# Kernel optimization log

Hardware: AMD Instinct MI355X
Metric: run time of the kernel (lower is better)

The kernel has to match this reference:

```python
import jax, jax.numpy as jnp
import numpy as np

NUM_HEADS = 16


def _bayes_w(mu, rho, eps):
    # reparameterized weight sample: w = mu + softplus(rho) * eps
    return mu + jax.nn.softplus(rho) * eps


def setup_inputs() -> dict:
    key = jax.random.key(0)
    ks = jax.random.split(key, 12)
    B, N, C = 4, 2048, 1024
    x = jax.random.normal(ks[0], (B, N, C), jnp.float32)
    w_scale = 0.02
    q_w = jax.random.normal(ks[1], (C, C), jnp.float32) * w_scale
    k_w = jax.random.normal(ks[2], (C, C), jnp.float32) * w_scale
    v_mu = jax.random.normal(ks[3], (C, C), jnp.float32) * w_scale
    v_rho = jax.random.normal(ks[4], (C, C), jnp.float32) * 0.1 - 3.0
    v_eps = jax.random.normal(ks[5], (C, C), jnp.float32)
    proj_mu = jax.random.normal(ks[6], (C, C), jnp.float32) * w_scale
    proj_rho = jax.random.normal(ks[7], (C, C), jnp.float32) * 0.1 - 3.0
    proj_eps = jax.random.normal(ks[8], (C, C), jnp.float32)
    pb_mu = jax.random.normal(ks[9], (C,), jnp.float32) * w_scale
    pb_rho = jax.random.normal(ks[10], (C,), jnp.float32) * 0.1 - 3.0
    pb_eps = jax.random.normal(ks[11], (C,), jnp.float32)
    return {"x": x, "q_w": q_w, "k_w": k_w, "v_mu": v_mu, "v_rho": v_rho,
            "v_eps": v_eps, "proj_mu": proj_mu, "proj_rho": proj_rho,
            "proj_eps": proj_eps, "pb_mu": pb_mu, "pb_rho": pb_rho,
            "pb_eps": pb_eps}


def reference(x, q_w, k_w, v_mu, v_rho, v_eps, proj_mu, proj_rho, proj_eps,
              pb_mu, pb_rho, pb_eps):
    B, N, C = x.shape
    H = NUM_HEADS
    D = C // H
    scale = D ** -0.5
    v_w = _bayes_w(v_mu, v_rho, v_eps)
    # projections (torch Linear: y = x @ W.T)
    q = (x @ q_w.T).reshape(B, N, H, D).transpose(0, 2, 1, 3)  # [B,H,N,D]
    k = (x @ k_w.T).reshape(B, N, H, D).transpose(0, 2, 1, 3)
    v = (x @ v_w.T).reshape(B, N, H, D).transpose(0, 2, 1, 3)
    attn = jax.nn.softmax(jnp.einsum("bhnd,bhmd->bhnm", q * scale, k), axis=-1)
    out = jnp.einsum("bhnm,bhmd->bhnd", attn, v)
    out = out.transpose(0, 2, 1, 3).reshape(B, N, C)
    p_w = _bayes_w(proj_mu, proj_rho, proj_eps)
    p_b = _bayes_w(pb_mu, pb_rho, pb_eps)
    return out @ p_w.T + p_b
```

## Files before the change

kernel.cpp:

```cpp
#include <hip/hip_runtime.h>
#include <hip/hip_bf16.h>
#include <cstdint>
#include <math.h>

typedef __bf16 bf16;
typedef __bf16 bf16x8 __attribute__((ext_vector_type(8)));
typedef __bf16 bf16x4 __attribute__((ext_vector_type(4)));
typedef float  f32x4 __attribute__((ext_vector_type(4)));

#define LOG2E 1.4426950408889634f

#if __has_builtin(__builtin_amdgcn_exp2f)
#define EXP2(x) __builtin_amdgcn_exp2f(x)
#else
#define EXP2(x) exp2f(x)
#endif

#define AS1 __attribute__((address_space(1)))
#define AS3 __attribute__((address_space(3)))

__device__ __forceinline__ void gload_lds16(const bf16* g, bf16* l) {
    __builtin_amdgcn_global_load_lds((AS1 void*)g, (AS3 void*)l, 16, 0, 0);
}

__device__ __forceinline__ float softplus_f(float r) {
    return (r > 15.f) ? r : log1pf(expf(r));
}

#define MFMA16(a, b, c) __builtin_amdgcn_mfma_f32_16x16x32_bf16((a), (b), (c), 0, 0, 0)
#define CFENCE asm volatile("" ::: "memory")

__global__ __launch_bounds__(256)
void prep_kernel(const float* __restrict__ x, bf16* __restrict__ xb,
                 const float* __restrict__ q_w, const float* __restrict__ k_w,
                 bf16* __restrict__ wqkv,
                 const float* __restrict__ v_mu, const float* __restrict__ v_rho,
                 const float* __restrict__ v_eps,
                 const float* __restrict__ p_mu, const float* __restrict__ p_rho,
                 const float* __restrict__ p_eps, bf16* __restrict__ pwb,
                 const float* __restrict__ pb_mu, const float* __restrict__ pb_rho,
                 const float* __restrict__ pb_eps, float* __restrict__ p_b) {
    const int Wsz = 1024 * 1024;
    int blk = blockIdx.x;
    if (blk < 8192) {
        int i = blk * 256 + threadIdx.x;
        float4 v = ((const float4*)x)[i];
        bf16 o[4] = {(bf16)v.x, (bf16)v.y, (bf16)v.z, (bf16)v.w};
        *(uint64_t*)&xb[i * 4] = *(uint64_t*)o;
    } else if (blk < 10240) {
        const float* src = (blk < 9216) ? q_w : k_w;
        bf16* dst = (blk < 9216) ? wqkv : wqkv + Wsz;
        int i = ((blk - 8192) & 1023) * 256 + threadIdx.x;
        float4 v = ((const float4*)src)[i];
        bf16 o[4] = {(bf16)v.x, (bf16)v.y, (bf16)v.z, (bf16)v.w};
        *(uint64_t*)&dst[i * 4] = *(uint64_t*)o;
    } else if (blk < 12288) {
        const bool isv = blk < 11264;
        const float* mu  = isv ? v_mu  : p_mu;
        const float* rho = isv ? v_rho : p_rho;
        const float* eps = isv ? v_eps : p_eps;
        bf16* dst = isv ? wqkv + 2 * Wsz : pwb;
        int i = ((blk - 10240) & 1023) * 256 + threadIdx.x;
        float4 m = ((const float4*)mu)[i];
        float4 r = ((const float4*)rho)[i];
        float4 e = ((const float4*)eps)[i];
        bf16 o[4] = {(bf16)(m.x + softplus_f(r.x) * e.x),
                     (bf16)(m.y + softplus_f(r.y) * e.y),
                     (bf16)(m.z + softplus_f(r.z) * e.z),
                     (bf16)(m.w + softplus_f(r.w) * e.w)};
        *(uint64_t*)&dst[i * 4] = *(uint64_t*)o;
    } else {
        int i = threadIdx.x;
        float4 m = ((const float4*)pb_mu)[i];
        float4 r = ((const float4*)pb_rho)[i];
        float4 e = ((const float4*)pb_eps)[i];
        float4 o;
        o.x = m.x + softplus_f(r.x) * e.x;
        o.y = m.y + softplus_f(r.y) * e.y;
        o.z = m.z + softplus_f(r.z) * e.z;
        o.w = m.w + softplus_f(r.w) * e.w;
        ((float4*)p_b)[i] = o;
    }
}

template <typename OutT, int BL>
__global__ __launch_bounds__(512, 2)
void gemm_8ph(const bf16* __restrict__ A, const bf16* __restrict__ W,
              OutT* __restrict__ C, const float* __restrict__ bias,
              int M, int N, int K, float q_scale, int q_cols) {
    __shared__ __align__(16) char smem[131072];
    bf16* sA = (bf16*)smem;
    bf16* sB = (bf16*)(smem + 65536);
    const int BN = 128 * BL;
    const int SBB = BN * 64;

    const int lane  = threadIdx.x & 63;
    const int wv    = threadIdx.x >> 6;
    const int wr    = wv >> 2;
    const int wc    = wv & 3;
    const int col16 = lane & 15, quad = lane >> 4;

    const int nwg = gridDim.x * gridDim.y;
    int bidl = blockIdx.y * gridDim.x + blockIdx.x;
    if ((nwg & 7) == 0) bidl = (bidl & 7) * (nwg >> 3) + (bidl >> 3);
    const int m0 = (bidl / gridDim.x) * 256;
    const int n0 = (bidl % gridDim.x) * BN;

    const int st_r = lane >> 2;
    const int st_c = ((lane & 3) * 8) ^ (((lane >> 5) & 1) << 4);
    const bf16* Asrc = A + (size_t)(m0 + st_r) * K + st_c;
    const bf16* Bsrc = W + (size_t)(n0 + st_r) * K + st_c;
    const size_t rgK = (size_t)16 * K;

    const int lp = col16 * 32 + ((quad * 8) ^ (((col16 >> 3) & 1) << 4));

    f32x4 acc[2][2][4][BL] = {};
    const int NT = K >> 6;

#define STAGE_A(buf, half, kt) do { \
        const bf16* s_ = Asrc + (size_t)((half) * 8 + wv) * rgK + ((size_t)(kt) << 6); \
        bf16* l_ = &sA[(buf) * 16384 + ((half) * 8 + wv) * 1024]; \
        gload_lds16(s_, l_); gload_lds16(s_ + 32, l_ + 512); } while (0)
#define STAGE_B(buf, half, kt) do { \
        if constexpr (BL == 2) { \
            const bf16* s_ = Bsrc + (size_t)((half) * 8 + wv) * rgK + ((size_t)(kt) << 6); \
            bf16* l_ = &sB[(buf) * SBB + ((half) * 8 + wv) * 1024]; \
            gload_lds16(s_, l_); gload_lds16(s_ + 32, l_ + 512); \
        } else { \
            const int rg_ = wv >> 1, kc_ = wv & 1; \
            const bf16* s_ = Bsrc + (size_t)((half) * 4 + rg_) * rgK + kc_ * 32 + ((size_t)(kt) << 6); \
            gload_lds16(s_, &sB[(buf) * SBB + (((half) * 4 + rg_) * 2 + kc_) * 512]); \
        } } while (0)
#define WAIT_STEADY do { \
        if constexpr (BL == 2) asm volatile("s_waitcnt vmcnt(6)" ::: "memory"); \
        else                   asm volatile("s_waitcnt vmcnt(4)" ::: "memory"); } while (0)

    STAGE_A(0, 0, 0); STAGE_B(0, 0, 0); STAGE_B(0, 1, 0); STAGE_A(0, 1, 0);
    if (NT > 1) { STAGE_A(1, 0, 1); STAGE_B(1, 0, 1); STAGE_B(1, 1, 1); }
    if (NT > 1) WAIT_STEADY;
    else        asm volatile("s_waitcnt vmcnt(0)" ::: "memory");
    __builtin_amdgcn_s_barrier();
    CFENCE;

    bf16x8 afr[4][2], bfr0[BL][2], bfr1[BL][2];

    for (int t = 0; t < NT; ++t) {
        const int d = t & 1;

#pragma unroll
        for (int mm = 0; mm < 4; ++mm)
#pragma unroll
            for (int ks = 0; ks < 2; ++ks)
                afr[mm][ks] = *(const bf16x8*)&sA[d * 16384 + ((2 * mm + wr) * 2 + ks) * 512 + lp];
#pragma unroll
        for (int nn = 0; nn < BL; ++nn)
#pragma unroll
            for (int ks = 0; ks < 2; ++ks)
                bfr0[nn][ks] = *(const bf16x8*)&sB[d * SBB + ((nn * 4 + wc) * 2 + ks) * 512 + lp];
        if (t + 1 < NT) STAGE_A(d ^ 1, 1, t + 1);
        CFENCE; __builtin_amdgcn_s_barrier(); CFENCE;
        __builtin_amdgcn_s_setprio(1);
#pragma unroll
        for (int mm = 0; mm < 4; ++mm)
#pragma unroll
            for (int nn = 0; nn < BL; ++nn) {
                acc[0][0][mm][nn] = MFMA16(afr[mm][0], bfr0[nn][0], acc[0][0][mm][nn]);
                acc[0][0][mm][nn] = MFMA16(afr[mm][1], bfr0[nn][1], acc[0][0][mm][nn]);
            }
        __builtin_amdgcn_s_setprio(0);
        CFENCE; __builtin_amdgcn_s_barrier(); CFENCE;

#pragma unroll
        for (int nn = 0; nn < BL; ++nn)
#pragma unroll
            for (int ks = 0; ks < 2; ++ks)
                bfr1[nn][ks] = *(const bf16x8*)&sB[d * SBB + ((4 * BL + nn * 4 + wc) * 2 + ks) * 512 + lp];
        if (t + 2 < NT) STAGE_A(d, 0, t + 2);
        CFENCE; __builtin_amdgcn_s_barrier(); CFENCE;
        __builtin_amdgcn_s_setprio(1);
#pragma unroll
        for (int mm = 0; mm < 4; ++mm)
#pragma unroll
            for (int nn = 0; nn < BL; ++nn) {
                acc[0][1][mm][nn] = MFMA16(afr[mm][0], bfr1[nn][0], acc[0][1][mm][nn]);
                acc[0][1][mm][nn] = MFMA16(afr[mm][1], bfr1[nn][1], acc[0][1][mm][nn]);
            }
        __builtin_amdgcn_s_setprio(0);
        CFENCE; __builtin_amdgcn_s_barrier(); CFENCE;

#pragma unroll
        for (int mm = 0; mm < 4; ++mm)
#pragma unroll
            for (int ks = 0; ks < 2; ++ks)
                afr[mm][ks] = *(const bf16x8*)&sA[d * 16384 + ((8 + 2 * mm + wr) * 2 + ks) * 512 + lp];
        if (t + 2 < NT) STAGE_B(d, 0, t + 2);
        CFENCE; __builtin_amdgcn_s_barrier(); CFENCE;
        __builtin_amdgcn_s_setprio(1);
#pragma unroll
        for (int mm = 0; mm < 4; ++mm)
#pragma unroll
            for (int nn = 0; nn < BL; ++nn) {
                acc[1][1][mm][nn] = MFMA16(afr[mm][0], bfr1[nn][0], acc[1][1][mm][nn]);
                acc[1][1][mm][nn] = MFMA16(afr[mm][1], bfr1[nn][1], acc[1][1][mm][nn]);
            }
        __builtin_amdgcn_s_setprio(0);
        CFENCE; __builtin_amdgcn_s_barrier(); CFENCE;

        if (t + 2 < NT) STAGE_B(d, 1, t + 2);
        CFENCE; __builtin_amdgcn_s_barrier(); CFENCE;
        __builtin_amdgcn_s_setprio(1);
#pragma unroll
        for (int mm = 0; mm < 4; ++mm)
#pragma unroll
            for (int nn = 0; nn < BL; ++nn) {
                acc[1][0][mm][nn] = MFMA16(afr[mm][0], bfr0[nn][0], acc[1][0][mm][nn]);
                acc[1][0][mm][nn] = MFMA16(afr[mm][1], bfr0[nn][1], acc[1][0][mm][nn]);
            }
        __builtin_amdgcn_s_setprio(0);
        if (t + 2 < NT) WAIT_STEADY;
        else            asm volatile("s_waitcnt vmcnt(0)" ::: "memory");
        __builtin_amdgcn_s_barrier();
        CFENCE;
    }
#undef STAGE_A
#undef STAGE_B
#undef WAIT_STEADY

    const float scale = (n0 < q_cols) ? q_scale : 1.0f;
#pragma unroll
    for (int a = 0; a < 2; ++a)
#pragma unroll
        for (int b = 0; b < 2; ++b)
#pragma unroll
            for (int mm = 0; mm < 4; ++mm)
#pragma unroll
                for (int nn = 0; nn < BL; ++nn) {
                    const int cc = (b * 4 * BL + nn * 4 + wc) * 16 + col16;
                    const float bv = bias ? bias[n0 + cc] : 0.f;
                    const int cb = cc * (int)sizeof(OutT);
#pragma unroll
                    for (int r = 0; r < 4; ++r) {
                        const int R = (a * 8 + 2 * mm + wr) * 16 + quad * 4 + r;
                        *(OutT*)(smem + R * 512 + (cb ^ ((R & 7) << 4))) =
                            (OutT)(acc[a][b][mm][nn][r] * scale + bv);
                    }
                }
    __syncthreads();
    char* Cb = (char*)C + ((size_t)m0 * N + n0) * sizeof(OutT);
    const size_t rowB = (size_t)N * sizeof(OutT);
    const int rr  = threadIdx.x >> 5;
    const int cb0 = (threadIdx.x & 31) * 16;
#pragma unroll
    for (int j = 0; j < 16; ++j) {
        const int R = j * 16 + rr;
        uint4 v = *(const uint4*)(smem + R * 512 + (cb0 ^ ((R & 7) << 4)));
        *(uint4*)(Cb + (size_t)R * rowB + cb0) = v;
    }
}

#define SWZ(row, ec) ((row) * 64 + ((ec) ^ (((row) & 7) << 3)))

__global__ __launch_bounds__(256, 2)
void attn_kernel(const bf16* __restrict__ QKV, bf16* __restrict__ O) {
    __shared__ bf16 sK[2][64 * 64];
    __shared__ bf16 sVt[64 * 64];
    __shared__ bf16 sP [256 * 64];

    const int lane = threadIdx.x & 63;
    const int wv   = threadIdx.x >> 6;
    const int col  = lane & 15, quad = lane >> 4;

    const int bid  = blockIdx.x;
    const int work = (bid & 7) * 64 + (bid >> 3);
    const int qt = work & 7, h = (work >> 3) & 15, b = work >> 7;

    const size_t rowQ0 = (size_t)b * 2048 + qt * 256;
    const bf16* Qg = QKV + rowQ0 * 3072 + h * 64;
    const bf16* Kg = QKV + (size_t)b * 2048 * 3072 + 1024 + h * 64;
    const bf16* Vg = QKV + (size_t)b * 2048 * 3072 + 2048 + h * 64;

    const int rloc = lane >> 3;
    const bf16* Kdma = Kg + (size_t)(wv * 16 + rloc) * 3072 + (((lane & 7) ^ rloc) * 8);

    gload_lds16(Kdma,                    &sK[0][(wv * 16) * 64]);
    gload_lds16(Kdma + (size_t)8 * 3072, &sK[0][(wv * 16 + 8) * 64]);

    const int dc0 = wv * 8, dc1 = 32 + wv * 8;
    bf16x8 vr0 = *(const bf16x8*)&Vg[(size_t)lane * 3072 + dc0];
    bf16x8 vr1 = *(const bf16x8*)&Vg[(size_t)lane * 3072 + dc1];

#pragma unroll
    for (int it = 0; it < 8; ++it) {
        int c = it * 256 + threadIdx.x;
        int row = c >> 3, ec = (c & 7) * 8;
        *(bf16x8*)&sP[SWZ(row, ec)] = *(const bf16x8*)&Qg[(size_t)row * 3072 + ec];
    }
    __syncthreads();
    bf16x8 qf[4][2];
#pragma unroll
    for (int mi = 0; mi < 4; ++mi)
#pragma unroll
        for (int ks = 0; ks < 2; ++ks)
            qf[mi][ks] = *(const bf16x8*)&sP[SWZ(wv * 64 + mi * 16 + col, ks * 32 + quad * 8)];

    f32x4 lsum[4] = {};
    f32x4 o[4][4] = {};
    const int cx = col & 7;

    for (int t = 0; t < 32; ++t) {
        const int p = t & 1;

#pragma unroll
        for (int j = 0; j < 8; ++j) sVt[SWZ(dc0 + j, lane)] = vr0[j];
#pragma unroll
        for (int j = 0; j < 8; ++j) sVt[SWZ(dc1 + j, lane)] = vr1[j];
        __syncthreads();

        if (t < 31) {
            const bf16* kn = Kdma + (size_t)(t * 64 + 64) * 3072;
            gload_lds16(kn,                    &sK[p ^ 1][(wv * 16) * 64]);
            gload_lds16(kn + (size_t)8 * 3072, &sK[p ^ 1][(wv * 16 + 8) * 64]);
        }

        bf16x8 kf0[4], kf1[4];
#pragma unroll
        for (int nj = 0; nj < 4; ++nj) {
            kf0[nj] = *(const bf16x8*)&sK[p][(nj * 16 + col) * 64 + ((quad ^ cx) * 8)];
            kf1[nj] = *(const bf16x8*)&sK[p][(nj * 16 + col) * 64 + (((quad ^ cx) ^ 4) * 8)];
        }

#pragma unroll
        for (int mi = 0; mi < 4; ++mi) {
            f32x4 st[4];
            __builtin_amdgcn_s_setprio(1);
#pragma unroll
            for (int nj = 0; nj < 4; ++nj) {
                f32x4 tacc = {0.f, 0.f, 0.f, 0.f};
                tacc = MFMA16(kf0[nj], qf[mi][0], tacc);
                tacc = MFMA16(kf1[nj], qf[mi][1], tacc);
                st[nj] = tacc;
            }
            __builtin_amdgcn_s_setprio(0);
#pragma unroll
            for (int nj = 0; nj < 4; ++nj) {
                f32x4 pv;
#pragma unroll
                for (int r = 0; r < 4; ++r) pv[r] = EXP2(st[nj][r]);
                lsum[mi] += pv;
                bf16x4 pk = {(bf16)pv[0], (bf16)pv[1], (bf16)pv[2], (bf16)pv[3]};
                *(bf16x4*)&sP[SWZ(wv * 64 + mi * 16 + col, nj * 16 + quad * 4)] = pk;
            }
        }

        if (t < 31) {
            const bf16* vn = Vg + (size_t)(t * 64 + 64 + lane) * 3072;
            vr0 = *(const bf16x8*)&vn[dc0];
            vr1 = *(const bf16x8*)&vn[dc1];
        }

        __builtin_amdgcn_s_setprio(1);
#pragma unroll
        for (int ks = 0; ks < 2; ++ks) {
            bf16x8 pf[4];
#pragma unroll
            for (int mi = 0; mi < 4; ++mi)
                pf[mi] = *(const bf16x8*)&sP[SWZ(wv * 64 + mi * 16 + col, ks * 32 + quad * 8)];
#pragma unroll
            for (int dj = 0; dj < 4; ++dj) {
                bf16x8 vf = *(const bf16x8*)&sVt[SWZ(dj * 16 + col, ks * 32 + quad * 8)];
#pragma unroll
                for (int mi = 0; mi < 4; ++mi)
                    o[mi][dj] = MFMA16(pf[mi], vf, o[mi][dj]);
            }
        }
        __builtin_amdgcn_s_setprio(0);
        __syncthreads();
    }

#pragma unroll
    for (int mi = 0; mi < 4; ++mi) {
        float l = lsum[mi][0] + lsum[mi][1] + lsum[mi][2] + lsum[mi][3];
        l += __shfl_xor(l, 16, 64);
        l += __shfl_xor(l, 32, 64);
#pragma unroll
        for (int r = 0; r < 4; ++r) {
            float inv = 1.f / __shfl(l, quad * 4 + r, 64);
            size_t row = rowQ0 + wv * 64 + mi * 16 + quad * 4 + r;
#pragma unroll
            for (int dj = 0; dj < 4; ++dj)
                O[row * 1024 + h * 64 + dj * 16 + col] = (bf16)(o[mi][dj][r] * inv);
        }
    }
}

extern "C" void kernel_launch(void* const* d_in, const int* in_sizes, int n_in,
                              void* d_out, int out_size, void* d_ws, size_t ws_size,
                              hipStream_t stream) {
    const float* x      = (const float*)d_in[0];
    const float* q_w    = (const float*)d_in[1];
    const float* k_w    = (const float*)d_in[2];
    const float* v_mu   = (const float*)d_in[3];
    const float* v_rho  = (const float*)d_in[4];
    const float* v_eps  = (const float*)d_in[5];
    const float* p_mu   = (const float*)d_in[6];
    const float* p_rho  = (const float*)d_in[7];
    const float* p_eps  = (const float*)d_in[8];
    const float* pb_mu  = (const float*)d_in[9];
    const float* pb_rho = (const float*)d_in[10];
    const float* pb_eps = (const float*)d_in[11];
    float* out = (float*)d_out;

    const size_t MB = (size_t)1 << 20;
    char* ws = (char*)d_ws;
    bf16*  xb   = (bf16*)(ws);
    bf16*  wqkv = (bf16*)(ws + 16 * MB);
    bf16*  pwb  = (bf16*)(ws + 22 * MB);
    float* p_b  = (float*)(ws + 24 * MB);
    bf16*  QKV  = (bf16*)(ws + 25 * MB);
    bf16*  Ab   = xb;

    prep_kernel<<<12289, 256, 0, stream>>>(x, xb, q_w, k_w, wqkv,
                                           v_mu, v_rho, v_eps,
                                           p_mu, p_rho, p_eps, pwb,
                                           pb_mu, pb_rho, pb_eps, p_b);

    gemm_8ph<bf16, 2><<<dim3(12, 32), 512, 0, stream>>>(xb, wqkv, QKV, nullptr,
                                                        8192, 3072, 1024, 0.125f * LOG2E, 1024);

    attn_kernel<<<dim3(512), 256, 0, stream>>>(QKV, Ab);

    gemm_8ph<float, 1><<<dim3(8, 32), 512, 0, stream>>>(Ab, pwb, out, p_b,
                                                        8192, 1024, 1024, 1.0f, 1024);
}
```

Before: 291.3 us.

## Halve P scratch and split score tile to raise attention occupancy

The attention inner loop is split into two halves of 32 keys each. Scores for one half are computed across all four query sub-tiles, exponentiated, written to a P buffer half the previous size, then immediately consumed by the PV MFMAs. Q fragments are loaded straight from global memory instead of being staged through LDS. Launch bounds go from 2 to 4 blocks per SM, relying on the smaller LDS footprint. The risks are register spilling under the tighter bound and uncoalesced Q loads. Reusing sP between halves without an intervening barrier looks safe only because each wave touches only its own rows.

Result: slower. 660.2 us (+126.6%).

```diff
diff --git a/kernel.cpp b/kernel.cpp
--- a/kernel.cpp
+++ b/kernel.cpp
@@ -259,12 +259,13 @@
 }
 
 #define SWZ(row, ec) ((row) * 64 + ((ec) ^ (((row) & 7) << 3)))
-
-__global__ __launch_bounds__(256, 2)
+#define SWZP(row, ec) ((row) * 32 + ((ec) ^ ((((row) >> 1) & 3) << 3)))
+
+__global__ __launch_bounds__(256, 4)
 void attn_kernel(const bf16* __restrict__ QKV, bf16* __restrict__ O) {
     __shared__ bf16 sK[2][64 * 64];
     __shared__ bf16 sVt[64 * 64];
-    __shared__ bf16 sP [256 * 64];
+    __shared__ bf16 sP [256 * 32];
 
     const int lane = threadIdx.x & 63;
     const int wv   = threadIdx.x >> 6;
@@ -289,19 +290,12 @@
     bf16x8 vr0 = *(const bf16x8*)&Vg[(size_t)lane * 3072 + dc0];
     bf16x8 vr1 = *(const bf16x8*)&Vg[(size_t)lane * 3072 + dc1];
 
-#pragma unroll
-    for (int it = 0; it < 8; ++it) {
-        int c = it * 256 + threadIdx.x;
-        int row = c >> 3, ec = (c & 7) * 8;
-        *(bf16x8*)&sP[SWZ(row, ec)] = *(const bf16x8*)&Qg[(size_t)row * 3072 + ec];
-    }
-    __syncthreads();
     bf16x8 qf[4][2];
 #pragma unroll
     for (int mi = 0; mi < 4; ++mi)
 #pragma unroll
         for (int ks = 0; ks < 2; ++ks)
-            qf[mi][ks] = *(const bf16x8*)&sP[SWZ(wv * 64 + mi * 16 + col, ks * 32 + quad * 8)];
+            qf[mi][ks] = *(const bf16x8*)&Qg[(size_t)(wv * 64 + mi * 16 + col) * 3072 + ks * 32 + quad * 8];
 
     f32x4 lsum[4] = {};
     f32x4 o[4][4] = {};
@@ -330,50 +324,52 @@
         }
 
 #pragma unroll
-        for (int mi = 0; mi < 4; ++mi) {
-            f32x4 st[4];
+        for (int hh = 0; hh < 2; ++hh) {
+            f32x4 st[4][2];
             __builtin_amdgcn_s_setprio(1);
 #pragma unroll
-            for (int nj = 0; nj < 4; ++nj) {
-                f32x4 tacc = {0.f, 0.f, 0.f, 0.f};
-                tacc = MFMA16(kf0[nj], qf[mi][0], tacc);
-                tacc = MFMA16(kf1[nj], qf[mi][1], tacc);
-                st[nj] = tacc;
-            }
+            for (int mi = 0; mi < 4; ++mi)
+#pragma unroll
+                for (int njl = 0; njl < 2; ++njl) {
+                    const int nj = hh * 2 + njl;
+                    f32x4 tacc = {0.f, 0.f, 0.f, 0.f};
+                    tacc = MFMA16(kf0[nj], qf[mi][0], tacc);
+                    tacc = MFMA16(kf1[nj], qf[mi][1], tacc);
+                    st[mi][njl] = tacc;
+                }
             __builtin_amdgcn_s_setprio(0);
 #pragma unroll
-            for (int nj = 0; nj < 4; ++nj) {
-                f32x4 pv;
-#pragma unroll
-                for (int r = 0; r < 4; ++r) pv[r] = EXP2(st[nj][r]);
-                lsum[mi] += pv;
-                bf16x4 pk = {(bf16)pv[0], (bf16)pv[1], (bf16)pv[2], (bf16)pv[3]};
-                *(bf16x4*)&sP[SWZ(wv * 64 + mi * 16 + col, nj * 16 + quad * 4)] = pk;
-            }
-        }
-
-        if (t < 31) {
-            const bf16* vn = Vg + (size_t)(t * 64 + 64 + lane) * 3072;
-            vr0 = *(const bf16x8*)&vn[dc0];
-            vr1 = *(const bf16x8*)&vn[dc1];
-        }
-
-        __builtin_amdgcn_s_setprio(1);
-#pragma unroll
-        for (int ks = 0; ks < 2; ++ks) {
+            for (int mi = 0; mi < 4; ++mi)
+#pragma unroll
+                for (int njl = 0; njl < 2; ++njl) {
+                    f32x4 pv;
+#pragma unroll
+                    for (int r = 0; r < 4; ++r) pv[r] = EXP2(st[mi][njl][r]);
+                    lsum[mi] += pv;
+                    bf16x4 pk = {(bf16)pv[0], (bf16)pv[1], (bf16)pv[2], (bf16)pv[3]};
+                    *(bf16x4*)&sP[SWZP(wv * 64 + mi * 16 + col, njl * 16 + quad * 4)] = pk;
+                }
+
+            if (hh == 0 && t < 31) {
+                const bf16* vn = Vg + (size_t)(t * 64 + 64 + lane) * 3072;
+                vr0 = *(const bf16x8*)&vn[dc0];
+                vr1 = *(const bf16x8*)&vn[dc1];
+            }
+
             bf16x8 pf[4];
 #pragma unroll
             for (int mi = 0; mi < 4; ++mi)
-                pf[mi] = *(const bf16x8*)&sP[SWZ(wv * 64 + mi * 16 + col, ks * 32 + quad * 8)];
+                pf[mi] = *(const bf16x8*)&sP[SWZP(wv * 64 + mi * 16 + col, quad * 8)];
+            __builtin_amdgcn_s_setprio(1);
 #pragma unroll
             for (int dj = 0; dj < 4; ++dj) {
-                bf16x8 vf = *(const bf16x8*)&sVt[SWZ(dj * 16 + col, ks * 32 + quad * 8)];
+                bf16x8 vf = *(const bf16x8*)&sVt[SWZ(dj * 16 + col, hh * 32 + quad * 8)];
 #pragma unroll
                 for (int mi = 0; mi < 4; ++mi)
                     o[mi][dj] = MFMA16(pf[mi], vf, o[mi][dj]);
             }
+            __builtin_amdgcn_s_setprio(0);
         }
-        __builtin_amdgcn_s_setprio(0);
         __syncthreads();
     }
 
```
